# Performance work log

Hardware: AMD Instinct MI355X
Metric: run time of the kernel (lower is better)

Reference implementation:

```python
import jax, jax.numpy as jnp
from jax import lax
import numpy as np

HEADS = 3
DIM_HEAD = 64
INNER = HEADS * DIM_HEAD  # 192
SCALE = DIM_HEAD ** -0.5
BN_EPS = 1e-5


def _sep_conv(x, dw, gamma, beta, mean, var, pw, stride):
    """Depthwise conv (SAME) -> BatchNorm (inference) -> 1x1 pointwise conv."""
    C = x.shape[-1]
    x = lax.conv_general_dilated(
        x, dw, window_strides=(stride, stride), padding='SAME',
        dimension_numbers=('NHWC', 'HWIO', 'NHWC'), feature_group_count=C)
    x = (x - mean) * lax.rsqrt(var + BN_EPS) * gamma + beta
    return jnp.einsum('bhwc,cd->bhwd', x, pw)


def setup_inputs() -> dict:
    key = jax.random.key(0)
    ks = jax.random.split(key, 8)
    B, H, W, C = 8, 56, 56, 192
    return {
        'x': jax.random.normal(ks[0], (B, H, W, C), dtype=jnp.float32),
        'dw_q': jax.random.normal(ks[1], (3, 3, 1, C), dtype=jnp.float32) * 0.1,
        'q_gamma': jnp.ones((C,), jnp.float32),
        'q_beta': jnp.zeros((C,), jnp.float32),
        'q_mean': jnp.zeros((C,), jnp.float32),
        'q_var': jnp.ones((C,), jnp.float32),
        'pw_q': jax.random.normal(ks[2], (C, INNER), dtype=jnp.float32) / np.sqrt(C).astype(np.float32),
        'dw_kv': jax.random.normal(ks[3], (3, 3, 1, C), dtype=jnp.float32) * 0.1,
        'kv_gamma': jnp.ones((C,), jnp.float32),
        'kv_beta': jnp.zeros((C,), jnp.float32),
        'kv_mean': jnp.zeros((C,), jnp.float32),
        'kv_var': jnp.ones((C,), jnp.float32),
        'pw_kv': jax.random.normal(ks[4], (C, 2 * INNER), dtype=jnp.float32) / np.sqrt(C).astype(np.float32),
        'out_w': jax.random.normal(ks[5], (INNER, C), dtype=jnp.float32) / np.sqrt(INNER).astype(np.float32),
        'out_b': jnp.zeros((C,), jnp.float32),
    }


def reference(x, dw_q, q_gamma, q_beta, q_mean, q_var, pw_q,
              dw_kv, kv_gamma, kv_beta, kv_mean, kv_var, pw_kv,
              out_w, out_b):
    B, H, W, C = x.shape
    q = _sep_conv(x, dw_q, q_gamma, q_beta, q_mean, q_var, pw_q, 1)      # [B,H,W,INNER]
    kv = _sep_conv(x, dw_kv, kv_gamma, kv_beta, kv_mean, kv_var, pw_kv, 2)  # [B,H/2,W/2,2*INNER]
    k, v = jnp.split(kv, 2, axis=-1)

    def split_heads(t):
        b, h, w, _ = t.shape
        return t.reshape(b, h * w, HEADS, DIM_HEAD)

    q, k, v = split_heads(q), split_heads(k), split_heads(v)  # [B,N,h,d]
    scores = jnp.einsum('bihd,bjhd->bhij', q, k) * SCALE       # [B,h,Nq,Nkv]
    attn = jax.nn.softmax(scores, axis=-1)
    o = jnp.einsum('bhij,bjhd->bihd', attn, v)                 # [B,Nq,h,d]
    o = o.reshape(B, H, W, INNER)
    return jnp.einsum('bhwc,cd->bhwd', o, out_w) + out_b
```

## Files before the change

kernel.cpp:

```cpp
#include <hip/hip_runtime.h>
#include <hip/hip_bf16.h>

namespace {
constexpr int Bb = 8, Hh = 56, Ww = 56, Cc = 192;
constexpr int NQ  = Hh * Ww;
constexpr int NKV = 28 * 28;
constexpr float EPS = 1e-5f;
constexpr float QSCALE = 0.125f * 1.4426950408889634f;
}

typedef __attribute__((ext_vector_type(8))) short          bf16x8;
typedef __attribute__((ext_vector_type(4))) float          f32x4;
typedef __attribute__((ext_vector_type(8))) unsigned short u16x8;

__device__ inline unsigned short f2b(float f) {
  __hip_bfloat16 h = __float2bfloat16(f);
  return __builtin_bit_cast(unsigned short, h);
}

__device__ inline uint2 pack4(float a, float b, float c, float d) {
  uint2 r;
  r.x = (unsigned)f2b(a) | ((unsigned)f2b(b) << 16);
  r.y = (unsigned)f2b(c) | ((unsigned)f2b(d) << 16);
  return r;
}

__device__ inline void dwbn_body(
    int idx, const float* __restrict__ x, const float* __restrict__ w,
    const float* __restrict__ gamma, const float* __restrict__ beta,
    const float* __restrict__ mean, const float* __restrict__ var,
    unsigned short* __restrict__ out, int OH, int OW, int stride, int pad)
{
  int c4 = idx % 48;
  int t = idx / 48;
  int ow = t % OW; t /= OW;
  int oh = t % OH; int b = t / OH;
  const int c = c4 * 4;

  float4 acc = make_float4(0.f, 0.f, 0.f, 0.f);
#pragma unroll
  for (int kh = 0; kh < 3; ++kh) {
    int ih = oh * stride - pad + kh;
    if (ih < 0 || ih >= Hh) continue;
#pragma unroll
    for (int kw = 0; kw < 3; ++kw) {
      int iw = ow * stride - pad + kw;
      if (iw < 0 || iw >= Ww) continue;
      float4 xv = *(const float4*)&x[((size_t)(b * Hh + ih) * Ww + iw) * Cc + c];
      float4 wv = *(const float4*)&w[(kh * 3 + kw) * Cc + c];
      acc.x += xv.x * wv.x; acc.y += xv.y * wv.y;
      acc.z += xv.z * wv.z; acc.w += xv.w * wv.w;
    }
  }
  float4 gm = *(const float4*)&gamma[c];
  float4 bt = *(const float4*)&beta[c];
  float4 mn = *(const float4*)&mean[c];
  float4 vr = *(const float4*)&var[c];
  float r0 = (acc.x - mn.x) * gm.x / sqrtf(vr.x + EPS) + bt.x;
  float r1 = (acc.y - mn.y) * gm.y / sqrtf(vr.y + EPS) + bt.y;
  float r2 = (acc.z - mn.z) * gm.z / sqrtf(vr.z + EPS) + bt.z;
  float r3 = (acc.w - mn.w) * gm.w / sqrtf(vr.w + EPS) + bt.w;
  const size_t row = (size_t)(b * OH + oh) * OW + ow;
  *reinterpret_cast<uint2*>(&out[row * 192 + c]) = pack4(r0, r1, r2, r3);
}

__global__ __launch_bounds__(256) void stage1_kernel(
    const float* __restrict__ x,
    const float* __restrict__ dw_q, const float* __restrict__ q_gamma,
    const float* __restrict__ q_beta, const float* __restrict__ q_mean,
    const float* __restrict__ q_var,
    const float* __restrict__ dw_kv, const float* __restrict__ kv_gamma,
    const float* __restrict__ kv_beta, const float* __restrict__ kv_mean,
    const float* __restrict__ kv_var,
    const float* __restrict__ pwq, const float* __restrict__ pwkv,
    const float* __restrict__ outw,
    unsigned short* __restrict__ dwq, unsigned short* __restrict__ dwkv,
    unsigned short* __restrict__ wq, unsigned short* __restrict__ wkv,
    unsigned short* __restrict__ wo)
{
  const int blk = blockIdx.x;
  if (blk < 4704) {
    dwbn_body(blk * 256 + threadIdx.x, x, dw_q, q_gamma, q_beta, q_mean, q_var,
              dwq, 56, 56, 1, 1);
  } else if (blk < 5880) {
    dwbn_body((blk - 4704) * 256 + threadIdx.x, x, dw_kv, kv_gamma, kv_beta,
              kv_mean, kv_var, dwkv, 28, 28, 2, 0);
  } else {
    int i = (blk - 5880) * 256 + threadIdx.x;
    if (i < 36864) {
      int n = i / 192, k = i - n * 192;
      wq[i] = f2b(pwq[k * 192 + n]);
    } else if (i < 110592) {
      int j = i - 36864;
      int n = j / 192, k = j - n * 192;
      wkv[j] = f2b(pwkv[k * 384 + n]);
    } else {
      int j = i - 110592;
      int n = j / 192, k = j - n * 192;
      wo[j] = f2b(outw[k * 192 + n]);
    }
  }
}

__global__ __launch_bounds__(256) void gemm_qkv_kernel(
    const unsigned short* __restrict__ dwq, const unsigned short* __restrict__ dwkv,
    const unsigned short* __restrict__ Wq, const unsigned short* __restrict__ Wkv,
    unsigned short* __restrict__ Qbuf, unsigned short* __restrict__ Kbuf,
    unsigned short* __restrict__ Vtbuf)
{
  __shared__ unsigned short As[128][72];
  __shared__ unsigned short Bs[64][72];

  const int blk = blockIdx.x;
  const bool isQ = blk < 588;
  const int lb = isQ ? blk : blk - 588;
  const unsigned short* __restrict__ A  = isQ ? dwq : dwkv;
  const unsigned short* __restrict__ Bt = isQ ? Wq : Wkv;
  const int nbl = isQ ? 3 : 6;
  const int NR  = isQ ? 3136 : 784;

  const int bm = lb / nbl, bn = lb % nbl;
  const int row0 = bm << 7, col0 = bn << 6;
  const int tid = threadIdx.x;
  const int lane = tid & 63, w = tid >> 6;
  const int lr = lane & 15, lg = lane >> 4;
  const int wm = w >> 1, wn = w & 1;

  f32x4 acc[4][2];
#pragma unroll
  for (int mr = 0; mr < 4; ++mr)
#pragma unroll
    for (int nr = 0; nr < 2; ++nr) acc[mr][nr] = (f32x4){0.f, 0.f, 0.f, 0.f};

  for (int k0 = 0; k0 < 192; k0 += 64) {
    {
      const int r = tid >> 1, c0 = (tid & 1) * 32;
      const unsigned short* src = A + (size_t)(row0 + r) * 192 + k0 + c0;
#pragma unroll
      for (int u = 0; u < 4; ++u)
        *(u16x8*)&As[r][c0 + u * 8] = *(const u16x8*)&src[u * 8];
    }
    {
      const int n = tid >> 2, c0 = (tid & 3) * 16;
      const unsigned short* src = Bt + (size_t)(col0 + n) * 192 + k0 + c0;
#pragma unroll
      for (int u = 0; u < 2; ++u)
        *(u16x8*)&Bs[n][c0 + u * 8] = *(const u16x8*)&src[u * 8];
    }
    __syncthreads();
#pragma unroll
    for (int ks = 0; ks < 2; ++ks) {
      bf16x8 a[4], b[2];
#pragma unroll
      for (int mr = 0; mr < 4; ++mr)
        a[mr] = *(const bf16x8*)&As[wm * 64 + mr * 16 + lr][ks * 32 + lg * 8];
#pragma unroll
      for (int nr = 0; nr < 2; ++nr)
        b[nr] = *(const bf16x8*)&Bs[wn * 32 + nr * 16 + lr][ks * 32 + lg * 8];
#pragma unroll
      for (int mr = 0; mr < 4; ++mr)
#pragma unroll
        for (int nr = 0; nr < 2; ++nr)
          acc[mr][nr] = __builtin_amdgcn_mfma_f32_16x16x32_bf16(a[mr], b[nr], acc[mr][nr], 0, 0, 0);
    }
    __syncthreads();
  }

#pragma unroll
  for (int mr = 0; mr < 4; ++mr) {
#pragma unroll
    for (int nr = 0; nr < 2; ++nr) {
      const int c = col0 + wn * 32 + nr * 16 + lr;
      const int rbase = row0 + wm * 64 + mr * 16 + lg * 4;
      if (isQ) {
        const int h = c >> 6, d = c & 63;
        const int b = rbase / 3136;
        const int n0 = rbase - b * 3136;
#pragma unroll
        for (int j = 0; j < 4; ++j)
          Qbuf[(((size_t)b * 3 + h) * 3136 + n0 + j) * 64 + d] = f2b(acc[mr][nr][j] * QSCALE);
      } else if (c < 192) {
        const int h = c >> 6, d = c & 63;
        const int b = rbase / 784;
        const int n0 = rbase - b * 784;
#pragma unroll
        for (int j = 0; j < 4; ++j)
          Kbuf[(((size_t)b * 3 + h) * 784 + n0 + j) * 64 + d] = f2b(acc[mr][nr][j]);
      } else {
        const int h = (c - 192) >> 6, d = (c - 192) & 63;
        const int b = rbase / 784;
        const int n0 = rbase - b * 784;
        uint2 v = pack4(acc[mr][nr][0], acc[mr][nr][1], acc[mr][nr][2], acc[mr][nr][3]);
        *reinterpret_cast<uint2*>(&Vtbuf[(((size_t)b * 3 + h) * 64 + d) * 784 + n0]) = v;
      }
    }
  }
}

__global__ __launch_bounds__(256) void gemm_out_kernel(
    const unsigned short* __restrict__ A, const unsigned short* __restrict__ Bt,
    const float* __restrict__ bias, float* __restrict__ O32)
{
  __shared__ unsigned short As[128][72];
  __shared__ unsigned short Bs[64][72];

  const int bm = blockIdx.x / 3, bn = blockIdx.x % 3;
  const int row0 = bm << 7, col0 = bn << 6;
  const int tid = threadIdx.x;
  const int lane = tid & 63, w = tid >> 6;
  const int lr = lane & 15, lg = lane >> 4;
  const int wm = w >> 1, wn = w & 1;

  f32x4 acc[4][2];
#pragma unroll
  for (int mr = 0; mr < 4; ++mr)
#pragma unroll
    for (int nr = 0; nr < 2; ++nr) acc[mr][nr] = (f32x4){0.f, 0.f, 0.f, 0.f};

  for (int k0 = 0; k0 < 192; k0 += 64) {
    {
      const int r = tid >> 1, c0 = (tid & 1) * 32;
      const unsigned short* src = A + (size_t)(row0 + r) * 192 + k0 + c0;
#pragma unroll
      for (int u = 0; u < 4; ++u)
        *(u16x8*)&As[r][c0 + u * 8] = *(const u16x8*)&src[u * 8];
    }
    {
      const int n = tid >> 2, c0 = (tid & 3) * 16;
      const unsigned short* src = Bt + (size_t)(col0 + n) * 192 + k0 + c0;
#pragma unroll
      for (int u = 0; u < 2; ++u)
        *(u16x8*)&Bs[n][c0 + u * 8] = *(const u16x8*)&src[u * 8];
    }
    __syncthreads();
#pragma unroll
    for (int ks = 0; ks < 2; ++ks) {
      bf16x8 a[4], b[2];
#pragma unroll
      for (int mr = 0; mr < 4; ++mr)
        a[mr] = *(const bf16x8*)&As[wm * 64 + mr * 16 + lr][ks * 32 + lg * 8];
#pragma unroll
      for (int nr = 0; nr < 2; ++nr)
        b[nr] = *(const bf16x8*)&Bs[wn * 32 + nr * 16 + lr][ks * 32 + lg * 8];
#pragma unroll
      for (int mr = 0; mr < 4; ++mr)
#pragma unroll
        for (int nr = 0; nr < 2; ++nr)
          acc[mr][nr] = __builtin_amdgcn_mfma_f32_16x16x32_bf16(a[mr], b[nr], acc[mr][nr], 0, 0, 0);
    }
    __syncthreads();
  }

#pragma unroll
  for (int mr = 0; mr < 4; ++mr) {
#pragma unroll
    for (int nr = 0; nr < 2; ++nr) {
      const int c = col0 + wn * 32 + nr * 16 + lr;
      const int rbase = row0 + wm * 64 + mr * 16 + lg * 4;
      const float bb = bias[c];
#pragma unroll
      for (int j = 0; j < 4; ++j)
        O32[(size_t)(rbase + j) * 192 + c] = acc[mr][nr][j] + bb;
    }
  }
}

__global__ __launch_bounds__(256) void attn_mfma_kernel(
    const unsigned short* __restrict__ Qb, const unsigned short* __restrict__ Kb,
    const unsigned short* __restrict__ Vtb, unsigned short* __restrict__ Ob)
{
  __shared__ unsigned short Ks[64][72];
  __shared__ unsigned short Vts[64][72];
  __shared__ unsigned short Ps[64][72];
  __shared__ float ls[4][16];

  const int raw = blockIdx.x;
  const int blk = (raw & 7) * 147 + (raw >> 3);
  const int qt = blk % 49;
  const int bh = blk / 49;
  const int n0 = qt * 64;
  const int tid = threadIdx.x;
  const int lane = tid & 63;
  const int w = tid >> 6;
  const int lr = lane & 15, lg = lane >> 4;
  const int srow = w * 16 + lr;
  const int scc  = lg;

  const unsigned short* qrow = Qb + ((size_t)bh * NQ + n0 + w * 16 + lr) * 64;
  const bf16x8 aq0 = *(const bf16x8*)&qrow[lg * 8];
  const bf16x8 aq1 = *(const bf16x8*)&qrow[32 + lg * 8];

  const unsigned short* kbase = Kb + (size_t)bh * NKV * 64;
  const unsigned short* vrow  = Vtb + ((size_t)bh * 64 + srow) * NKV;

  u16x8 kr0, kr1, vr0, vr1;
  {
    const unsigned short* kp = kbase + (size_t)srow * 64;
    kr0 = *(const u16x8*)&kp[scc * 8];
    kr1 = *(const u16x8*)&kp[scc * 8 + 32];
    vr0 = *(const u16x8*)&vrow[scc * 8];
    vr1 = *(const u16x8*)&vrow[scc * 8 + 32];
  }
  *(u16x8*)&Ks[srow][scc * 8]       = kr0;
  *(u16x8*)&Ks[srow][scc * 8 + 32]  = kr1;
  *(u16x8*)&Vts[srow][scc * 8]      = vr0;
  *(u16x8*)&Vts[srow][scc * 8 + 32] = vr1;
  __syncthreads();

  f32x4 oacc[4];
#pragma unroll
  for (int db = 0; db < 4; ++db) oacc[db] = (f32x4){0.f, 0.f, 0.f, 0.f};
  float lsum = 0.f;

  for (int kt = 0; kt < 12; ++kt) {
    {
      const int nk = kt + 1;
      const int kvg = (nk * 64 + srow < NKV) ? nk * 64 + srow : NKV - 1;
      const unsigned short* kp = kbase + (size_t)kvg * 64;
      kr0 = *(const u16x8*)&kp[scc * 8];
      kr1 = *(const u16x8*)&kp[scc * 8 + 32];
      const int vb = nk * 64 + scc * 8;
      const int vc0 = (vb      <= NKV - 8) ? vb      : NKV - 8;
      const int vc1 = (vb + 32 <= NKV - 8) ? vb + 32 : NKV - 8;
      vr0 = *(const u16x8*)&vrow[vc0];
      vr1 = *(const u16x8*)&vrow[vc1];
    }

    f32x4 st[4];
    __builtin_amdgcn_s_setprio(1);
#pragma unroll
    for (int nb = 0; nb < 4; ++nb) {
      const bf16x8 bk0 = *(const bf16x8*)&Ks[nb * 16 + lr][lg * 8];
      const bf16x8 bk1 = *(const bf16x8*)&Ks[nb * 16 + lr][32 + lg * 8];
      f32x4 a = (f32x4){0.f, 0.f, 0.f, 0.f};
      a = __builtin_amdgcn_mfma_f32_16x16x32_bf16(bk0, aq0, a, 0, 0, 0);
      a = __builtin_amdgcn_mfma_f32_16x16x32_bf16(bk1, aq1, a, 0, 0, 0);
      st[nb] = a;
    }
    __builtin_amdgcn_s_setprio(0);

#pragma unroll
    for (int nb = 0; nb < 4; ++nb) {
      float p[4];
#pragma unroll
      for (int r = 0; r < 4; ++r) p[r] = exp2f(st[nb][r]);
      lsum += (p[0] + p[1]) + (p[2] + p[3]);
      uint2 u = pack4(p[0], p[1], p[2], p[3]);
      *reinterpret_cast<uint2*>(&Ps[w * 16 + lr][nb * 16 + lg * 4]) = u;
    }

    const bf16x8 pa0 = *(const bf16x8*)&Ps[w * 16 + lr][lg * 8];
    const bf16x8 pa1 = *(const bf16x8*)&Ps[w * 16 + lr][32 + lg * 8];
    __builtin_amdgcn_s_setprio(1);
#pragma unroll
    for (int db = 0; db < 4; ++db) {
      const bf16x8 vb0 = *(const bf16x8*)&Vts[db * 16 + lr][lg * 8];
      const bf16x8 vb1 = *(const bf16x8*)&Vts[db * 16 + lr][32 + lg * 8];
      oacc[db] = __builtin_amdgcn_mfma_f32_16x16x32_bf16(pa0, vb0, oacc[db], 0, 0, 0);
      oacc[db] = __builtin_amdgcn_mfma_f32_16x16x32_bf16(pa1, vb1, oacc[db], 0, 0, 0);
    }
    __builtin_amdgcn_s_setprio(0);

    __syncthreads();
    *(u16x8*)&Ks[srow][scc * 8]       = kr0;
    *(u16x8*)&Ks[srow][scc * 8 + 32]  = kr1;
    *(u16x8*)&Vts[srow][scc * 8]      = vr0;
    *(u16x8*)&Vts[srow][scc * 8 + 32] = vr1;
    __syncthreads();
  }

  {
    const bf16x8 bk0 = *(const bf16x8*)&Ks[lr][lg * 8];
    const bf16x8 bk1 = *(const bf16x8*)&Ks[lr][32 + lg * 8];
    f32x4 a = (f32x4){0.f, 0.f, 0.f, 0.f};
    a = __builtin_amdgcn_mfma_f32_16x16x32_bf16(bk0, aq0, a, 0, 0, 0);
    a = __builtin_amdgcn_mfma_f32_16x16x32_bf16(bk1, aq1, a, 0, 0, 0);
    float p[4];
#pragma unroll
    for (int r = 0; r < 4; ++r) p[r] = exp2f(a[r]);
    lsum += (p[0] + p[1]) + (p[2] + p[3]);
    *reinterpret_cast<uint2*>(&Ps[w * 16 + lr][lg * 4]) = pack4(p[0], p[1], p[2], p[3]);
    uint2 z; z.x = 0u; z.y = 0u;
    *reinterpret_cast<uint2*>(&Ps[w * 16 + lr][16 + lg * 4]) = z;
    const bf16x8 pa0 = *(const bf16x8*)&Ps[w * 16 + lr][lg * 8];
#pragma unroll
    for (int db = 0; db < 4; ++db) {
      const bf16x8 vb0 = *(const bf16x8*)&Vts[db * 16 + lr][lg * 8];
      oacc[db] = __builtin_amdgcn_mfma_f32_16x16x32_bf16(pa0, vb0, oacc[db], 0, 0, 0);
    }
  }

  float l = lsum;
  l += __shfl_xor(l, 16);
  l += __shfl_xor(l, 32);
  if (lg == 0) ls[w][lr] = l;
  const float4 lv = *(const float4*)&ls[w][lg * 4];

  const int b = bh / 3, h = bh - b * 3;
  float linv[4];
#pragma unroll
  for (int j = 0; j < 4; ++j) linv[j] = 1.f / ((&lv.x)[j]);
#pragma unroll
  for (int j = 0; j < 4; ++j) {
    const int qg = n0 + w * 16 + lg * 4 + j;
    unsigned short* orow = Ob + ((size_t)b * NQ + qg) * 192 + h * 64 + lr;
#pragma unroll
    for (int db = 0; db < 4; ++db) orow[db * 16] = f2b(oacc[db][j] * linv[j]);
  }
}

extern "C" void kernel_launch(void* const* d_in, const int* in_sizes, int n_in,
                              void* d_out, int out_size, void* d_ws, size_t ws_size,
                              hipStream_t stream)
{
  const float* x        = (const float*)d_in[0];
  const float* dw_q     = (const float*)d_in[1];
  const float* q_gamma  = (const float*)d_in[2];
  const float* q_beta   = (const float*)d_in[3];
  const float* q_mean   = (const float*)d_in[4];
  const float* q_var    = (const float*)d_in[5];
  const float* pw_q     = (const float*)d_in[6];
  const float* dw_kv    = (const float*)d_in[7];
  const float* kv_gamma = (const float*)d_in[8];
  const float* kv_beta  = (const float*)d_in[9];
  const float* kv_mean  = (const float*)d_in[10];
  const float* kv_var   = (const float*)d_in[11];
  const float* pw_kv    = (const float*)d_in[12];
  const float* out_w    = (const float*)d_in[13];
  const float* out_b    = (const float*)d_in[14];
  float* out = (float*)d_out;

  unsigned short* dwq   = (unsigned short*)d_ws;
  unsigned short* dwkv  = dwq   + (size_t)25088 * 192;
  unsigned short* Qbuf  = dwkv  + (size_t)6272 * 192;
  unsigned short* Kbuf  = Qbuf  + (size_t)24 * 3136 * 64;
  unsigned short* Vtbuf = Kbuf  + (size_t)24 * 784 * 64;
  unsigned short* Wq    = Vtbuf + (size_t)24 * 784 * 64;
  unsigned short* Wkv   = Wq + 36864;
  unsigned short* Wo    = Wkv + 73728;

  stage1_kernel<<<6456, 256, 0, stream>>>(
      x, dw_q, q_gamma, q_beta, q_mean, q_var,
      dw_kv, kv_gamma, kv_beta, kv_mean, kv_var,
      pw_q, pw_kv, out_w, dwq, dwkv, Wq, Wkv, Wo);
  gemm_qkv_kernel<<<882, 256, 0, stream>>>(dwq, dwkv, Wq, Wkv, Qbuf, Kbuf, Vtbuf);
  attn_mfma_kernel<<<8 * 3 * 49, 256, 0, stream>>>(Qbuf, Kbuf, Vtbuf, dwq);
  gemm_out_kernel<<<588, 256, 0, stream>>>(dwq, Wo, out_b, out);
}
```

Before: 91.42 us.

## Double-buffer K/V tiles in attention and remap GEMM blocks across XCDs

The attention kernel now keeps two LDS buffers for K and V^T. Each iteration writes the next tile into the spare buffer and needs one barrier instead of two. Both GEMM kernels also remap blockIdx so that consecutive logical tiles land on the same XCD, which should improve L2 locality on the 8-XCD part. The cost is extra LDS per block, which may lower occupancy.

```diff
diff --git a/kernel.cpp b/kernel.cpp
--- a/kernel.cpp
+++ b/kernel.cpp
@@ -111,7 +111,9 @@
   __shared__ unsigned short As[128][72];
   __shared__ unsigned short Bs[64][72];
 
-  const int blk = blockIdx.x;
+  const int raw = blockIdx.x;
+  const int x8 = raw & 7, ci = raw >> 3;
+  const int blk = (x8 < 2 ? x8 * 111 : 222 + (x8 - 2) * 110) + ci;
   const bool isQ = blk < 588;
   const int lb = isQ ? blk : blk - 588;
   const unsigned short* __restrict__ A  = isQ ? dwq : dwkv;
@@ -204,7 +206,10 @@
   __shared__ unsigned short As[128][72];
   __shared__ unsigned short Bs[64][72];
 
-  const int bm = blockIdx.x / 3, bn = blockIdx.x % 3;
+  const int raw = blockIdx.x;
+  const int x8 = raw & 7, ci = raw >> 3;
+  const int blk = (x8 < 4 ? x8 * 74 : 296 + (x8 - 4) * 73) + ci;
+  const int bm = blk / 3, bn = blk % 3;
   const int row0 = bm << 7, col0 = bn << 6;
   const int tid = threadIdx.x;
   const int lane = tid & 63, w = tid >> 6;
@@ -269,8 +274,8 @@
     const unsigned short* __restrict__ Qb, const unsigned short* __restrict__ Kb,
     const unsigned short* __restrict__ Vtb, unsigned short* __restrict__ Ob)
 {
-  __shared__ unsigned short Ks[64][72];
-  __shared__ unsigned short Vts[64][72];
+  __shared__ unsigned short Ks[2][64][72];
+  __shared__ unsigned short Vts[2][64][72];
   __shared__ unsigned short Ps[64][72];
   __shared__ float ls[4][16];
 
@@ -301,10 +306,10 @@
     vr0 = *(const u16x8*)&vrow[scc * 8];
     vr1 = *(const u16x8*)&vrow[scc * 8 + 32];
   }
-  *(u16x8*)&Ks[srow][scc * 8]       = kr0;
-  *(u16x8*)&Ks[srow][scc * 8 + 32]  = kr1;
-  *(u16x8*)&Vts[srow][scc * 8]      = vr0;
-  *(u16x8*)&Vts[srow][scc * 8 + 32] = vr1;
+  *(u16x8*)&Ks[0][srow][scc * 8]       = kr0;
+  *(u16x8*)&Ks[0][srow][scc * 8 + 32]  = kr1;
+  *(u16x8*)&Vts[0][srow][scc * 8]      = vr0;
+  *(u16x8*)&Vts[0][srow][scc * 8 + 32] = vr1;
   __syncthreads();
 
   f32x4 oacc[4];
@@ -312,6 +317,7 @@
   for (int db = 0; db < 4; ++db) oacc[db] = (f32x4){0.f, 0.f, 0.f, 0.f};
   float lsum = 0.f;
 
+  int cur = 0;
   for (int kt = 0; kt < 12; ++kt) {
     {
       const int nk = kt + 1;
@@ -330,8 +336,8 @@
     __builtin_amdgcn_s_setprio(1);
 #pragma unroll
     for (int nb = 0; nb < 4; ++nb) {
-      const bf16x8 bk0 = *(const bf16x8*)&Ks[nb * 16 + lr][lg * 8];
-      const bf16x8 bk1 = *(const bf16x8*)&Ks[nb * 16 + lr][32 + lg * 8];
+      const bf16x8 bk0 = *(const bf16x8*)&Ks[cur][nb * 16 + lr][lg * 8];
+      const bf16x8 bk1 = *(const bf16x8*)&Ks[cur][nb * 16 + lr][32 + lg * 8];
       f32x4 a = (f32x4){0.f, 0.f, 0.f, 0.f};
       a = __builtin_amdgcn_mfma_f32_16x16x32_bf16(bk0, aq0, a, 0, 0, 0);
       a = __builtin_amdgcn_mfma_f32_16x16x32_bf16(bk1, aq1, a, 0, 0, 0);
@@ -354,24 +360,24 @@
     __builtin_amdgcn_s_setprio(1);
 #pragma unroll
     for (int db = 0; db < 4; ++db) {
-      const bf16x8 vb0 = *(const bf16x8*)&Vts[db * 16 + lr][lg * 8];
-      const bf16x8 vb1 = *(const bf16x8*)&Vts[db * 16 + lr][32 + lg * 8];
+      const bf16x8 vb0 = *(const bf16x8*)&Vts[cur][db * 16 + lr][lg * 8];
+      const bf16x8 vb1 = *(const bf16x8*)&Vts[cur][db * 16 + lr][32 + lg * 8];
       oacc[db] = __builtin_amdgcn_mfma_f32_16x16x32_bf16(pa0, vb0, oacc[db], 0, 0, 0);
       oacc[db] = __builtin_amdgcn_mfma_f32_16x16x32_bf16(pa1, vb1, oacc[db], 0, 0, 0);
     }
     __builtin_amdgcn_s_setprio(0);
 
+    *(u16x8*)&Ks[cur ^ 1][srow][scc * 8]       = kr0;
+    *(u16x8*)&Ks[cur ^ 1][srow][scc * 8 + 32]  = kr1;
+    *(u16x8*)&Vts[cur ^ 1][srow][scc * 8]      = vr0;
+    *(u16x8*)&Vts[cur ^ 1][srow][scc * 8 + 32] = vr1;
     __syncthreads();
-    *(u16x8*)&Ks[srow][scc * 8]       = kr0;
-    *(u16x8*)&Ks[srow][scc * 8 + 32]  = kr1;
-    *(u16x8*)&Vts[srow][scc * 8]      = vr0;
-    *(u16x8*)&Vts[srow][scc * 8 + 32] = vr1;
-    __syncthreads();
+    cur ^= 1;
   }
 
   {
-    const bf16x8 bk0 = *(const bf16x8*)&Ks[lr][lg * 8];
-    const bf16x8 bk1 = *(const bf16x8*)&Ks[lr][32 + lg * 8];
+    const bf16x8 bk0 = *(const bf16x8*)&Ks[cur][lr][lg * 8];
+    const bf16x8 bk1 = *(const bf16x8*)&Ks[cur][lr][32 + lg * 8];
     f32x4 a = (f32x4){0.f, 0.f, 0.f, 0.f};
     a = __builtin_amdgcn_mfma_f32_16x16x32_bf16(bk0, aq0, a, 0, 0, 0);
     a = __builtin_amdgcn_mfma_f32_16x16x32_bf16(bk1, aq1, a, 0, 0, 0);
@@ -385,7 +391,7 @@
     const bf16x8 pa0 = *(const bf16x8*)&Ps[w * 16 + lr][lg * 8];
 #pragma unroll
     for (int db = 0; db < 4; ++db) {
-      const bf16x8 vb0 = *(const bf16x8*)&Vts[db * 16 + lr][lg * 8];
+      const bf16x8 vb0 = *(const bf16x8*)&Vts[cur][db * 16 + lr][lg * 8];
       oacc[db] = __builtin_amdgcn_mfma_f32_16x16x32_bf16(pa0, vb0, oacc[db], 0, 0, 0);
     }
   }
```

New measurement: 90.28 us. About the same (-1.2%).
